# Optimization experiments

Measured on AMD Instinct MI355X. Metric: run time of the kernel, lower is better.

## Reference

```python
import jax, jax.numpy as jnp
import numpy as np

N, F, E = 2048, 4, 65536
D, H, FF = 256, 4, 2048  # d_model, n_heads, transformer feedforward dim
HD = D // H


def setup_inputs() -> dict:
    key = jax.random.key(0)
    ks = jax.random.split(key, 26)
    p = lambda k, shape, fan_in: (jax.random.normal(k, shape, jnp.float32) / np.sqrt(fan_in))
    return {
        "features": jax.random.normal(ks[0], (N, F), jnp.float32),
        "edges": jax.random.randint(ks[1], (2, E), 0, N, jnp.int64),
        # Embedder.linear: Linear(1, 256)
        "lin_w": p(ks[2], (D, 1), 1), "lin_b": jnp.zeros((D,), jnp.float32),
        # TransformerEncoderLayer self-attention
        "in_proj_w": p(ks[3], (3 * D, D), D), "in_proj_b": jnp.zeros((3 * D,), jnp.float32),
        "out_w": p(ks[4], (D, D), D), "out_b": jnp.zeros((D,), jnp.float32),
        "ln1_g": jnp.ones((D,), jnp.float32), "ln1_b": jnp.zeros((D,), jnp.float32),
        # feedforward
        "ffn_w1": p(ks[5], (FF, D), D), "ffn_b1": jnp.zeros((FF,), jnp.float32),
        "ffn_w2": p(ks[6], (D, FF), FF), "ffn_b2": jnp.zeros((D,), jnp.float32),
        "ln2_g": jnp.ones((D,), jnp.float32), "ln2_b": jnp.zeros((D,), jnp.float32),
        # 4 GCNConv layers (torch Linear convention: weight [out, in])
        "W1": p(ks[7], (512, D), D), "b1": jnp.zeros((512,), jnp.float32),
        "W2": p(ks[8], (512, 512), 512), "b2": jnp.zeros((512,), jnp.float32),
        "W3": p(ks[9], (512, 512), 512), "b3": jnp.zeros((512,), jnp.float32),
        "W4": p(ks[10], (512, 512), 512), "b4": jnp.zeros((512,), jnp.float32),
    }


def _layer_norm(x, g, b, eps=1e-5):
    m = jnp.mean(x, axis=-1, keepdims=True)
    v = jnp.mean((x - m) ** 2, axis=-1, keepdims=True)
    return (x - m) / jnp.sqrt(v + eps) * g + b


def _gcn_conv(x, W, b, src, dst, n):
    # PyG GCNConv: h = x @ W^T; add self-loops; norm = deg^-1/2[src]*deg^-1/2[dst];
    # out = scatter_add(norm * h[src] -> dst) + bias
    h = x @ W.T
    loop = jnp.arange(n, dtype=src.dtype)
    s = jnp.concatenate([src, loop])
    d = jnp.concatenate([dst, loop])
    deg = jax.ops.segment_sum(jnp.ones_like(d, dtype=h.dtype), d, num_segments=n)
    dinv = jnp.where(deg > 0, deg ** -0.5, 0.0)
    norm = dinv[s] * dinv[d]
    return jax.ops.segment_sum(h[s] * norm[:, None], d, num_segments=n) + b


def reference(features, edges, lin_w, lin_b, in_proj_w, in_proj_b, out_w, out_b,
              ln1_g, ln1_b, ffn_w1, ffn_b1, ffn_w2, ffn_b2, ln2_g, ln2_b,
              W1, b1, W2, b2, W3, b3, W4, b4):
    n, f = features.shape
    # Embedder: [N,F,1] -> Linear(1,D) -> [N,F,D]; seq-first transformer (seq=N, batch=F)
    x = features[..., None] @ lin_w.T + lin_b  # [N,F,D]
    qkv = x @ in_proj_w.T + in_proj_b          # [N,F,3D]
    q, k, v = jnp.split(qkv, 3, axis=-1)
    split = lambda t: t.reshape(n, f, H, HD).transpose(1, 2, 0, 3)  # [F,H,N,hd]
    q, k, v = split(q), split(k), split(v)
    scores = jnp.einsum('bhqd,bhkd->bhqk', q, k) / np.sqrt(HD)      # [F,H,N,N]
    attn = jax.nn.softmax(scores, axis=-1)
    o = jnp.einsum('bhqk,bhkd->bhqd', attn, v).transpose(2, 0, 1, 3).reshape(n, f, D)
    o = o @ out_w.T + out_b
    x = _layer_norm(x + o, ln1_g, ln1_b)
    ff = jax.nn.relu(x @ ffn_w1.T + ffn_b1) @ ffn_w2.T + ffn_b2
    x = _layer_norm(x + ff, ln2_g, ln2_b)
    x = jax.nn.relu(jnp.mean(x, axis=1))  # mean over feature-batch dim -> [N,D]

    src, dst = edges[0], edges[1]
    x = jax.nn.relu(_gcn_conv(x, W1, b1, src, dst, n))
    x = jax.nn.relu(_gcn_conv(x, W2, b2, src, dst, n))
    x = jax.nn.relu(_gcn_conv(x, W3, b3, src, dst, n))
    x = _gcn_conv(x, W4, b4, src, dst, n)
    return x
```

## Files before the change

kernel.cpp:

```cpp
#include <hip/hip_runtime.h>
#include <hip/hip_bf16.h>
#include <math.h>

#define NN   2048
#define FB   4
#define DD   256
#define EE   65536
#define NT   (NN*FB)
#define FFD  2048

typedef unsigned int u32;
typedef unsigned short u16;
typedef __attribute__((ext_vector_type(4))) float f32x4;
typedef __attribute__((ext_vector_type(8))) short bf16x8;

#define OFF_W2   0
#define OFF_G1   524288
#define OFF_G2   655360
#define OFF_G3   917504
#define OFF_G4   1179648
#define WBF_TOT  1441792

__device__ float g_A[768], g_B[768];
__device__ float g_coefA[4], g_coefC[4];
__device__ float g_meanv[6], g_G[36];
__device__ float g_Vx[8*DD];
__device__ u16   g_w1vh[FFD*8];
__device__ float g_m[NT*4];
__device__ float g_cc[NT*8];
__device__ u16   g_xmh[NN*DD];
__device__ u16   g_hsh[NN*512];
__device__ u16   g_xgh[NN*512];
__device__ u16   g_wbf[WBF_TOT];
__device__ __align__(64) int g_degp[NN*16];
__device__ __align__(64) int g_curp[NN*16];
__device__ int   g_off[NN+1], g_adj[EE];
__device__ float g_dinv[NN];

__device__ __forceinline__ u16 f2bf(float x) {
  u32 u = __float_as_uint(x);
  return (u16)((u + 0x7FFFu + ((u >> 16) & 1u)) >> 16);
}
__device__ __forceinline__ float bfl(u32 v) { return __uint_as_float(v << 16); }
__device__ __forceinline__ float bfh(u32 v) { return __uint_as_float(v & 0xffff0000u); }
__device__ __forceinline__ void gl_lds16(const void* g, void* l) {
  __builtin_amdgcn_global_load_lds(
      (const __attribute__((address_space(1))) u32*)g,
      (__attribute__((address_space(3))) u32*)l, 16, 0, 0);
}
__device__ __forceinline__ float qred(float v) {
  v += __shfl_xor(v, 1, 64);
  v += __shfl_xor(v, 2, 64);
  return v;
}
__device__ __forceinline__ void acc8(const uint4 v, float* a) {
  a[0]+=bfl(v.x); a[1]+=bfh(v.x);
  a[2]+=bfl(v.y); a[3]+=bfh(v.y);
  a[4]+=bfl(v.z); a[5]+=bfh(v.z);
  a[6]+=bfl(v.w); a[7]+=bfh(v.w);
}

__global__ __launch_bounds__(256) void k_fuse1(const float* __restrict__ ipw,
    const float* __restrict__ ipb, const float* __restrict__ linw,
    const float* __restrict__ linb) {
  __shared__ __align__(16) float sm[512];
  const int b = blockIdx.x, t = threadIdx.x;
  if (b < 12) {
    float* lw = sm; float* lb = sm + 256;
    lw[t] = linw[t]; lb[t] = linb[t];
    __syncthreads();
    int j = b*64 + (t>>2), c = t&3;
    const float4* row = (const float4*)&ipw[j*256 + c*64];
    float a = 0.f, bb = 0.f;
    #pragma unroll
    for (int q = 0; q < 16; q++) {
      float4 v = row[q]; int d0 = c*64 + q*4;
      a  += v.x*lw[d0] + v.y*lw[d0+1] + v.z*lw[d0+2] + v.w*lw[d0+3];
      bb += v.x*lb[d0] + v.y*lb[d0+1] + v.z*lb[d0+2] + v.w*lb[d0+3];
    }
    a = qred(a); bb = qred(bb);
    if (c == 0) { g_A[j] = a; g_B[j] = bb + ipb[j]; }
  } else {
    int i = (b - 12)*256 + t;
    if (i < NN*16) { g_degp[i] = 0; g_curp[i] = 0; }
  }
}

__global__ __launch_bounds__(256) void k_fuse2(const float* __restrict__ outw,
    const float* __restrict__ outb, const float* __restrict__ linw,
    const float* __restrict__ linb, const float* __restrict__ g1,
    const float* __restrict__ b1ln, const int* __restrict__ edges) {
  __shared__ __align__(16) float sm[512 + 4*27];
  const int b = blockIdx.x, t = threadIdx.x;
  if (b == 0) {
    int lane = t & 63, w = t >> 6;
    {
      float aq = g_A[w*64 + lane], ak = g_A[256 + w*64 + lane], bq = g_B[w*64 + lane];
      float pa = aq * ak, pc = bq * ak;
      #pragma unroll
      for (int o = 32; o > 0; o >>= 1) { pa += __shfl_down(pa, o, 64); pc += __shfl_down(pc, o, 64); }
      if (lane == 0) { g_coefA[w] = pa * 0.125f; g_coefC[w] = pc * 0.125f; }
    }
    float* A2 = sm; float* B2 = sm + 256; float* wred = sm + 512;
    A2[t] = g_A[512 + t]; B2[t] = g_B[512 + t];
    __syncthreads();
    const int d = t;
    const float4* row = (const float4*)&outw[d*256];
    float pv[4] = {0,0,0,0}, q0 = 0.f;
    #pragma unroll 8
    for (int q = 0; q < 64; q++) {
      float4 v = row[q]; int e0 = q*4; int h = q >> 4;
      pv[h] += v.x*A2[e0] + v.y*A2[e0+1] + v.z*A2[e0+2] + v.w*A2[e0+3];
      q0    += v.x*B2[e0] + v.y*B2[e0+1] + v.z*B2[e0+2] + v.w*B2[e0+3];
    }
    q0 += outb[d];
    float c0 = linb[d] + q0;
    float Mv[6] = { linw[d], pv[0], pv[1], pv[2], pv[3], c0 };
    float vals[27];
    { int idx = 0;
      #pragma unroll
      for (int k = 0; k < 6; k++) vals[idx++] = Mv[k];
      #pragma unroll
      for (int k = 0; k < 6; k++)
        #pragma unroll
        for (int l = 0; l < 6; l++) if (l >= k) vals[idx++] = Mv[k]*Mv[l];
    }
    #pragma unroll
    for (int k2 = 0; k2 < 27; k2++) {
      float v = vals[k2];
      #pragma unroll
      for (int o = 32; o > 0; o >>= 1) v += __shfl_down(v, o, 64);
      if (lane == 0) wred[w*27 + k2] = v;
    }
    __syncthreads();
    if (t < 27) {
      float s = wred[t] + wred[27 + t] + wred[54 + t] + wred[81 + t];
      if (t < 6) g_meanv[t] = s * (1.f/256.f);
      else {
        int p = t - 6, k = 0;
        while (p >= 6 - k) { p -= 6 - k; k++; }
        int l = k + p;
        g_G[k*6+l] = s; g_G[l*6+k] = s;
      }
    }
    #pragma unroll
    for (int k = 0; k < 6; k++) g_Vx[k*256 + d] = Mv[k] * g1[d];
    g_Vx[6*256 + d] = g1[d];
    g_Vx[7*256 + d] = b1ln[d];
  } else {
    int e = (b - 1)*256 + t;
    atomicAdd(&g_degp[edges[EE + e] * 16], 1);
  }
}

__global__ __launch_bounds__(256) void k_fuse3(const float* __restrict__ feat,
    const float* __restrict__ w1, const float* __restrict__ fb1,
    const float* __restrict__ w2c, const float* __restrict__ W1c,
    const float* __restrict__ W2c, const float* __restrict__ W3c,
    const float* __restrict__ W4c) {
  __shared__ __align__(16) char smraw[34816];
  const int b = blockIdx.x, t = threadIdx.x;
  if (b < 512) {
    float* fs = (float*)smraw;
    float* ss = fs + 8192;
    float* ww = ss + 256;
    for (int i = t; i < 2048; i += 256) {
      const float4 v = *(const float4*)&feat[i*4];
      fs[0*2048+i] = v.x; fs[1*2048+i] = v.y; fs[2*2048+i] = v.z; fs[3*2048+i] = v.w;
    }
    __syncthreads();
    int tuple = b * 64 + (t >> 2);
    int c = t & 3;
    int h = tuple & 3, f = (tuple >> 2) & 3, n = tuple >> 4;
    float fi = fs[f*2048 + n];
    float tt = g_coefA[h] * fi + g_coefC[h];
    float s = 0.f, wsum = 0.f;
    int j0 = c * 512;
    for (int j = j0; j < j0 + 512; j++) {
      float fj = fs[f*2048 + j];
      float e = __expf(tt * fj);
      s += e; wsum += e * fj;
    }
    ss[(t>>2)*4 + c] = s; ww[(t>>2)*4 + c] = wsum;
    __syncthreads();
    if (c == 0) {
      float S = ss[(t>>2)*4] + ss[(t>>2)*4+1] + ss[(t>>2)*4+2] + ss[(t>>2)*4+3];
      float W = ww[(t>>2)*4] + ww[(t>>2)*4+1] + ww[(t>>2)*4+2] + ww[(t>>2)*4+3];
      g_m[tuple] = W / S;
    }
  } else if (b < 544) {
    float* vx = (float*)smraw;
    #pragma unroll
    for (int k = 0; k < 8; k++) vx[k*256 + t] = g_Vx[k*256 + t];
    __syncthreads();
    int j = (b - 512)*64 + (t>>2), c = t&3;
    const float4* row = (const float4*)&w1[j*256 + c*64];
    float acc[8] = {0,0,0,0,0,0,0,0};
    #pragma unroll
    for (int q = 0; q < 16; q++) {
      float4 v = row[q]; int d0 = c*64 + q*4;
      #pragma unroll
      for (int k = 0; k < 8; k++)
        acc[k] += v.x*vx[k*256+d0] + v.y*vx[k*256+d0+1]
                + v.z*vx[k*256+d0+2] + v.w*vx[k*256+d0+3];
    }
    #pragma unroll
    for (int k = 0; k < 8; k++) acc[k] = qred(acc[k]);
    if (c == 0) {
      acc[7] += fb1[j];
      uint4 r;
      r.x = ((u32)f2bf(acc[1])<<16) | f2bf(acc[0]);
      r.y = ((u32)f2bf(acc[3])<<16) | f2bf(acc[2]);
      r.z = ((u32)f2bf(acc[5])<<16) | f2bf(acc[4]);
      r.w = ((u32)f2bf(acc[7])<<16) | f2bf(acc[6]);
      *(uint4*)&g_w1vh[j*8] = r;
    }
  } else if (b == 544) {
    int* wt = (int*)smraw;
    int base = t * 8;
    int v[8], ex[8], sum = 0;
    #pragma unroll
    for (int i = 0; i < 8; i++) { ex[i] = sum; v[i] = g_degp[(base+i)*16]; sum += v[i]; }
    int lane = t & 63, w = t >> 6;
    int inc = sum;
    #pragma unroll
    for (int o = 1; o < 64; o <<= 1) { int x = __shfl_up(inc, o, 64); if (lane >= o) inc += x; }
    if (lane == 63) wt[w] = inc;
    __syncthreads();
    int wb = 0;
    for (int j = 0; j < w; j++) wb += wt[j];
    int excl = wb + inc - sum;
    #pragma unroll
    for (int i = 0; i < 8; i++) {
      g_off[base+i] = excl + ex[i];
      g_dinv[base+i] = rsqrtf((float)(v[i] + 1));
    }
    if (t == 255) g_off[NN] = wb + inc;
  } else {
    int i = ((b - 545)*256 + t) * 4;
    const float* src; int off;
    if (i < OFF_G1)      { src = w2c; off = OFF_W2; }
    else if (i < OFF_G2) { src = W1c; off = OFF_G1; }
    else if (i < OFF_G3) { src = W2c; off = OFF_G2; }
    else if (i < OFF_G4) { src = W3c; off = OFF_G3; }
    else                 { src = W4c; off = OFF_G4; }
    float4 v = *(const float4*)&src[i - off];
    ushort4 r;
    r.x = f2bf(v.x); r.y = f2bf(v.y); r.z = f2bf(v.z); r.w = f2bf(v.w);
    *(ushort4*)&g_wbf[i] = r;
  }
}

__global__ __launch_bounds__(256) void k_fuse4(const float* __restrict__ feat,
                                               const int* __restrict__ edges) {
  const int b = blockIdx.x, t = threadIdx.x;
  if (b < 32) {
    int tok = b * 256 + t;
    int n = tok >> 2, f = tok & 3;
    float fi = feat[n*4 + f];
    float u[6] = { fi, g_m[tok*4+0], g_m[tok*4+1], g_m[tok*4+2], g_m[tok*4+3], 1.f };
    float mu = 0.f;
    #pragma unroll
    for (int k = 0; k < 6; k++) mu += g_meanv[k] * u[k];
    float q = 0.f;
    for (int k = 0; k < 6; k++)
      for (int l = 0; l < 6; l++) q += u[k] * g_G[k*6+l] * u[l];
    q *= (1.f/256.f);
    float var = q - mu * mu;
    float s = rsqrtf(var + 1e-5f);
    float4 w0; w0.x = fi*s; w0.y = u[1]*s; w0.z = u[2]*s; w0.w = u[3]*s;
    float4 w1v; w1v.x = u[4]*s; w1v.y = s; w1v.z = -mu*s; w1v.w = 1.f;
    *(float4*)&g_cc[tok*8]     = w0;
    *(float4*)&g_cc[tok*8 + 4] = w1v;
  } else {
    int e = (b - 32)*256 + t;
    int s = edges[e], d = edges[EE + e];
    int pos = atomicAdd(&g_curp[d*16], 1);
    g_adj[g_off[d] + pos] = s;
  }
}

__global__ __launch_bounds__(256) void k_ffnln(const float* __restrict__ fb2,
    const float* __restrict__ ln2g, const float* __restrict__ ln2b) {
  __shared__ __align__(16) char smp[74752];
  u16*   Bsl  = (u16*)smp;
  u16*   Asl  = (u16*)(smp + 65536);
  u16*   w1sl = (u16*)(smp + 69632);
  float* ccs  = (float*)(smp + 73728);
  float* part = (float*)(smp + 74240);

  const int b = blockIdx.x, t = threadIdx.x;
  const int w = t >> 6, lane = t & 63, fr = lane & 15, gk = lane >> 4;
  const int tok0 = b * 16;
  const u16* W2p = g_wbf + OFF_W2;

  if (t < 32) ((float4*)ccs)[t] = ((const float4*)&g_cc[tok0*8])[t];
  if (w == 1) {
    #pragma unroll
    for (int hh = 0; hh < 2; hh++) {
      int p = hh*64 + lane;
      int q = (p & ~7) | ((p ^ (p >> 3)) & 7);
      gl_lds16(g_w1vh + (size_t)q*8, w1sl + (hh << 9));
    }
  }
  __syncthreads();

  const int arow = t >> 4, aslot = t & 15;
  float ac[8];
  #pragma unroll
  for (int k = 0; k < 8; k++) ac[k] = ccs[arow*8 + k];

  f32x4 acc[4] = {};
  for (int it = 0; it < 16; it++) {
    const int k0 = it << 7;
    const int cur = it & 1;
    #pragma unroll
    for (int c = 0; c < 16; c++) {
      int col0 = (w << 6) + (c << 2);
      int colL = col0 + (lane >> 4);
      int p = lane & 15;
      int q = (p & 8) | ((p ^ (colL & 7)) & 7);
      gl_lds16(W2p + (size_t)colL*FFD + k0 + q*8, Bsl + (col0 << 7));
    }
    if (w == 1 && it < 15) {
      #pragma unroll
      for (int hh = 0; hh < 2; hh++) {
        int p = hh*64 + lane;
        int q = (p & ~7) | ((p ^ (p >> 3)) & 7);
        gl_lds16(g_w1vh + (size_t)(k0 + 128 + q)*8, w1sl + ((cur ^ 1) << 10) + (hh << 9));
      }
    }
    {
      float h[8];
      #pragma unroll
      for (int e2 = 0; e2 < 8; e2++) {
        int ph = aslot*8 + (e2 ^ (aslot & 7));
        uint4 wv = *(const uint4*)&w1sl[(cur << 10) + ph*8];
        float s = ac[0]*bfl(wv.x) + ac[1]*bfh(wv.x)
                + ac[2]*bfl(wv.y) + ac[3]*bfh(wv.y)
                + ac[4]*bfl(wv.z) + ac[5]*bfh(wv.z)
                + ac[6]*bfl(wv.w) + ac[7]*bfh(wv.w);
        h[e2] = fmaxf(s, 0.f);
      }
      uint4 r;
      r.x = ((u32)f2bf(h[1])<<16) | f2bf(h[0]);
      r.y = ((u32)f2bf(h[3])<<16) | f2bf(h[2]);
      r.z = ((u32)f2bf(h[5])<<16) | f2bf(h[4]);
      r.w = ((u32)f2bf(h[7])<<16) | f2bf(h[6]);
      int ph = (aslot & 8) | ((aslot ^ (arow & 7)) & 7);
      *(uint4*)&Asl[(arow << 7) + (ph << 3)] = r;
    }
    __syncthreads();
    #pragma unroll
    for (int kk = 0; kk < 4; kk++) {
      int qa = (kk << 2) + gk;
      int pa = (qa & 8) | ((qa ^ (fr & 7)) & 7);
      bf16x8 af = *(const bf16x8*)&Asl[(fr << 7) + (pa << 3)];
      #pragma unroll
      for (int nb = 0; nb < 4; nb++) {
        int col = (w << 6) + (nb << 4) + fr;
        int pb = (qa & 8) | ((qa ^ (col & 7)) & 7);
        bf16x8 bv = *(const bf16x8*)&Bsl[(col << 7) + (pb << 3)];
        acc[nb] = __builtin_amdgcn_mfma_f32_16x16x32_bf16(af, bv, acc[nb], 0, 0, 0);
      }
    }
    __syncthreads();
  }

  #pragma unroll
  for (int nb = 0; nb < 4; nb++) {
    int col = (w << 6) + (nb << 4) + fr;
    float fb = fb2[col];
    #pragma unroll
    for (int r = 0; r < 4; r++) {
      int row = gk*4 + r;
      float x1 = 0.f;
      #pragma unroll
      for (int k = 0; k < 8; k++) x1 += ccs[row*8 + k] * g_Vx[k*256 + col];
      acc[nb][r] += fb + x1;
    }
  }
  float s1[4] = {0,0,0,0}, s2v[4] = {0,0,0,0};
  #pragma unroll
  for (int r = 0; r < 4; r++)
    #pragma unroll
    for (int nb = 0; nb < 4; nb++) {
      float v = acc[nb][r];
      s1[r] += v; s2v[r] += v*v;
    }
  #pragma unroll
  for (int o = 1; o < 16; o <<= 1) {
    #pragma unroll
    for (int r = 0; r < 4; r++) {
      s1[r]  += __shfl_xor(s1[r],  o, 64);
      s2v[r] += __shfl_xor(s2v[r], o, 64);
    }
  }
  if (fr == 0) {
    #pragma unroll
    for (int r = 0; r < 4; r++) {
      int row = gk*4 + r;
      part[(w*16 + row)*2 + 0] = s1[r];
      part[(w*16 + row)*2 + 1] = s2v[r];
    }
  }
  __syncthreads();
  float mu[4], inv[4];
  #pragma unroll
  for (int r = 0; r < 4; r++) {
    int row = gk*4 + r;
    float S1 = 0.f, S2 = 0.f;
    #pragma unroll
    for (int wv = 0; wv < 4; wv++) {
      S1 += part[(wv*16 + row)*2 + 0];
      S2 += part[(wv*16 + row)*2 + 1];
    }
    float m = S1 * (1.f/256.f);
    mu[r] = m;
    inv[r] = rsqrtf(S2 * (1.f/256.f) - m*m + 1e-5f);
  }
  const int node = b*4 + gk;
  #pragma unroll
  for (int nb = 0; nb < 4; nb++) {
    int col = (w << 6) + (nb << 4) + fr;
    float g = ln2g[col], bb = ln2b[col];
    float m = 0.f;
    #pragma unroll
    for (int r = 0; r < 4; r++)
      m += (acc[nb][r] - mu[r]) * inv[r] * g + bb;
    g_xmh[node*256 + col] = f2bf(fmaxf(m * 0.25f, 0.f));
  }
}

template<int DO_ROWSCALE, int OUT_BF16, int HAS_BIAS>
__global__ __launch_bounds__(256) void k_mm64(
    const u16* __restrict__ A, const u16* __restrict__ Bm, void* __restrict__ Cv,
    int M, int N, int K,
    const float* __restrict__ rowscale, const float* __restrict__ bias)
{
  __shared__ u16 Asl[32*64];
  __shared__ u16 Bsl[64*64];
  const int t = threadIdx.x;
  const int w = t >> 6, lane = t & 63;
  const int bm = blockIdx.y * 32, bn = blockIdx.x * 64;
  const int wr = w >> 1, wc = w & 1;
  const int fr = lane & 15;
  const int gk = lane >> 4;
  f32x4 acc[2] = {};
  for (int k0 = 0; k0 < K; k0 += 64) {
    {
      int r = (w << 3) + (lane >> 3);
      int ks = (((lane & 7) ^ (r & 7)) << 3);
      gl_lds16(A + (size_t)(bm + r)*K + k0 + ks, Asl + (w << 9));
    }
    #pragma unroll
    for (int c = 0; c < 2; c++) {
      int r2 = (w << 4) + (c << 3) + (lane >> 3);
      int ks2 = (((lane & 7) ^ (r2 & 7)) << 3);
      gl_lds16(Bm + (size_t)(bn + r2)*K + k0 + ks2, Bsl + (w << 10) + (c << 9));
    }
    __syncthreads();
    bf16x8 af[2], bfv[2][2];
    #pragma unroll
    for (int kk = 0; kk < 2; kk++) {
      int q = (kk << 2) + gk;
      int row = wr*16 + fr;
      af[kk] = *(const bf16x8*)&Asl[(row << 6) + ((q ^ (row & 7)) << 3)];
    }
    #pragma unroll
    for (int nb = 0; nb < 2; nb++) {
      int col = wc*32 + nb*16 + fr;
      #pragma unroll
      for (int kk = 0; kk < 2; kk++) {
        int q = (kk << 2) + gk;
        bfv[nb][kk] = *(const bf16x8*)&Bsl[(col << 6) + ((q ^ (col & 7)) << 3)];
      }
    }
    #pragma unroll
    for (int kk = 0; kk < 2; kk++)
      #pragma unroll
      for (int nb = 0; nb < 2; nb++)
        acc[nb] = __builtin_amdgcn_mfma_f32_16x16x32_bf16(af[kk], bfv[nb][kk], acc[nb], 0, 0, 0);
    __syncthreads();
  }
  #pragma unroll
  for (int r = 0; r < 4; r++) {
    int row = bm + wr*16 + gk*4 + r;
    float rs = DO_ROWSCALE ? rowscale[row] : 1.f;
    #pragma unroll
    for (int nb = 0; nb < 2; nb++) {
      int col = bn + wc*32 + nb*16 + fr;
      float v = acc[nb][r];
      if (HAS_BIAS) v += bias[col];
      if (DO_ROWSCALE) v *= rs;
      if (OUT_BF16) ((u16*)Cv)[(size_t)row*N + col] = f2bf(v);
      else ((float*)Cv)[(size_t)row*N + col] = v;
    }
  }
}

template<int OUT_BF16, int DO_RELU>
__global__ __launch_bounds__(256) void k_agg(const float* __restrict__ bias,
                                             void* __restrict__ outv) {
  const int t = threadIdx.x, w = t >> 6, lane = t & 63;
  const int i = blockIdx.x*4 + w;
  const int d = lane * 8;
  const uint4* tbl = (const uint4*)g_hsh;
  float a[8] = {0,0,0,0,0,0,0,0};
  acc8(tbl[i*64 + lane], a);
  int e0 = g_off[i], e1 = g_off[i+1];
  int e = e0;
  for (; e + 4 <= e1; e += 4) {
    int s0 = g_adj[e+0], s1 = g_adj[e+1], s2 = g_adj[e+2], s3 = g_adj[e+3];
    uint4 v0 = tbl[s0*64 + lane];
    uint4 v1 = tbl[s1*64 + lane];
    uint4 v2 = tbl[s2*64 + lane];
    uint4 v3 = tbl[s3*64 + lane];
    acc8(v0, a); acc8(v1, a); acc8(v2, a); acc8(v3, a);
  }
  for (; e < e1; e++) acc8(tbl[g_adj[e]*64 + lane], a);
  float di = g_dinv[i];
  const float4 b0 = *(const float4*)&bias[d];
  const float4 b1 = *(const float4*)&bias[d+4];
  a[0]=di*a[0]+b0.x; a[1]=di*a[1]+b0.y; a[2]=di*a[2]+b0.z; a[3]=di*a[3]+b0.w;
  a[4]=di*a[4]+b1.x; a[5]=di*a[5]+b1.y; a[6]=di*a[6]+b1.z; a[7]=di*a[7]+b1.w;
  if (DO_RELU) {
    #pragma unroll
    for (int q = 0; q < 8; q++) a[q] = fmaxf(a[q], 0.f);
  }
  if (OUT_BF16) {
    uint4 r;
    r.x = ((u32)f2bf(a[1])<<16) | f2bf(a[0]);
    r.y = ((u32)f2bf(a[3])<<16) | f2bf(a[2]);
    r.z = ((u32)f2bf(a[5])<<16) | f2bf(a[4]);
    r.w = ((u32)f2bf(a[7])<<16) | f2bf(a[6]);
    *(uint4*)&((u16*)outv)[i*512 + d] = r;
  } else {
    float4 r0; r0.x=a[0]; r0.y=a[1]; r0.z=a[2]; r0.w=a[3];
    float4 r1; r1.x=a[4]; r1.y=a[5]; r1.z=a[6]; r1.w=a[7];
    *(float4*)&((float*)outv)[i*512 + d]     = r0;
    *(float4*)&((float*)outv)[i*512 + d + 4] = r1;
  }
}

static float* symf(const void* s) { void* p = nullptr; (void)hipGetSymbolAddress(&p, s); return (float*)p; }

extern "C" void kernel_launch(void* const* d_in, const int* in_sizes, int n_in,
                              void* d_out, int out_size, void* d_ws, size_t ws_size,
                              hipStream_t stream) {
  const float* feat = (const float*)d_in[0];
  const int*   edges= (const int*)  d_in[1];
  const float* linw = (const float*)d_in[2];
  const float* linb = (const float*)d_in[3];
  const float* ipw  = (const float*)d_in[4];
  const float* ipb  = (const float*)d_in[5];
  const float* outw = (const float*)d_in[6];
  const float* outb = (const float*)d_in[7];
  const float* ln1g = (const float*)d_in[8];
  const float* ln1b = (const float*)d_in[9];
  const float* fw1  = (const float*)d_in[10];
  const float* fb1  = (const float*)d_in[11];
  const float* fw2  = (const float*)d_in[12];
  const float* fb2  = (const float*)d_in[13];
  const float* ln2g = (const float*)d_in[14];
  const float* ln2b = (const float*)d_in[15];
  const float* W1g  = (const float*)d_in[16];
  const float* b1g  = (const float*)d_in[17];
  const float* W2g  = (const float*)d_in[18];
  const float* b2g  = (const float*)d_in[19];
  const float* W3g  = (const float*)d_in[20];
  const float* b3g  = (const float*)d_in[21];
  const float* W4g  = (const float*)d_in[22];
  const float* b4g  = (const float*)d_in[23];
  float* out = (float*)d_out;

  u16*   p_xmh = (u16*)symf(HIP_SYMBOL(g_xmh));
  u16*   p_hsh = (u16*)symf(HIP_SYMBOL(g_hsh));
  u16*   p_xgh = (u16*)symf(HIP_SYMBOL(g_xgh));
  u16*   p_wbf = (u16*)symf(HIP_SYMBOL(g_wbf));
  float* p_dinv= symf(HIP_SYMBOL(g_dinv));

  k_fuse1<<<140,  256, 0, stream>>>(ipw, ipb, linw, linb);
  k_fuse2<<<257,  256, 0, stream>>>(outw, outb, linw, linb, ln1g, ln1b, edges);
  k_fuse3<<<1953, 256, 0, stream>>>(feat, fw1, fb1, fw2, W1g, W2g, W3g, W4g);
  k_fuse4<<<288,  256, 0, stream>>>(feat, edges);

  k_ffnln<<<512, 256, 0, stream>>>(fb2, ln2g, ln2b);

  k_mm64<1,1,0><<<dim3(8, 64), 256, 0, stream>>>(
      p_xmh, p_wbf + OFF_G1, p_hsh, NN, 512, 256, p_dinv, nullptr);
  k_agg<1,1><<<NN/4, 256, 0, stream>>>(b1g, p_xgh);
  k_mm64<1,1,0><<<dim3(8, 64), 256, 0, stream>>>(
      p_xgh, p_wbf + OFF_G2, p_hsh, NN, 512, 512, p_dinv, nullptr);
  k_agg<1,1><<<NN/4, 256, 0, stream>>>(b2g, p_xgh);
  k_mm64<1,1,0><<<dim3(8, 64), 256, 0, stream>>>(
      p_xgh, p_wbf + OFF_G3, p_hsh, NN, 512, 512, p_dinv, nullptr);
  k_agg<1,1><<<NN/4, 256, 0, stream>>>(b3g, p_xgh);
  k_mm64<1,1,0><<<dim3(8, 64), 256, 0, stream>>>(
      p_xgh, p_wbf + OFF_G4, p_hsh, NN, 512, 512, p_dinv, nullptr);
  k_agg<0,0><<<NN/4, 256, 0, stream>>>(b4g, out);
}
```

Measured before the change: 166.4 us.

## Retile FFN to 64-token by 128-column blocks and split LayerNorm into separate kernel

The fused FFN+LayerNorm kernel is replaced by one that processes 64 tokens by 128 output columns per block (256 blocks instead of 512). The whole W1 vector table is preloaded into LDS, and each W2 tile load is reused across four times more tokens. Because the 256 LN columns are now split across two blocks, the kernel writes fp32 pre-norm activations and partial sums to global memory. A new k_ln2m kernel then applies LayerNorm2, the feature mean and ReLU. This cuts redundant W2 traffic and W1 reloads but adds an 8 MB fp32 round trip, an extra launch, fewer blocks, and larger LDS use per block.

```diff
diff --git a/kernel.cpp b/kernel.cpp
--- a/kernel.cpp
+++ b/kernel.cpp
@@ -28,6 +28,8 @@
 __device__ u16   g_w1vh[FFD*8];
 __device__ float g_m[NT*4];
 __device__ float g_cc[NT*8];
+__device__ float g_ffv[(size_t)NT*DD];
+__device__ float g_lnp[NT*2*2];
 __device__ u16   g_xmh[NN*DD];
 __device__ u16   g_hsh[NN*512];
 __device__ u16   g_xgh[NN*512];
@@ -280,86 +282,84 @@
   }
 }
 
-__global__ __launch_bounds__(256) void k_ffnln(const float* __restrict__ fb2,
-    const float* __restrict__ ln2g, const float* __restrict__ ln2b) {
-  __shared__ __align__(16) char smp[74752];
+__global__ __launch_bounds__(256) void k_ffn(const float* __restrict__ fb2) {
+  __shared__ __align__(16) char smp[88576];
   u16*   Bsl  = (u16*)smp;
-  u16*   Asl  = (u16*)(smp + 65536);
-  u16*   w1sl = (u16*)(smp + 69632);
-  float* ccs  = (float*)(smp + 73728);
-  float* part = (float*)(smp + 74240);
+  u16*   Asl  = (u16*)(smp + 32768);
+  u16*   w1s  = (u16*)(smp + 49152);
+  float* ccs  = (float*)(smp + 81920);
+  float* vxs  = (float*)(smp + 83968);
+  float* fb2s = (float*)(smp + 88064);
 
   const int b = blockIdx.x, t = threadIdx.x;
   const int w = t >> 6, lane = t & 63, fr = lane & 15, gk = lane >> 4;
-  const int tok0 = b * 16;
+  const int tb = b >> 1, ch = b & 1;
+  const int tok0 = tb * 64, gc0 = ch * 128;
   const u16* W2p = g_wbf + OFF_W2;
 
-  if (t < 32) ((float4*)ccs)[t] = ((const float4*)&g_cc[tok0*8])[t];
-  if (w == 1) {
-    #pragma unroll
-    for (int hh = 0; hh < 2; hh++) {
-      int p = hh*64 + lane;
-      int q = (p & ~7) | ((p ^ (p >> 3)) & 7);
-      gl_lds16(g_w1vh + (size_t)q*8, w1sl + (hh << 9));
-    }
-  }
+  #pragma unroll
+  for (int q = 0; q < 8; q++) {
+    int jj = t + q*256;
+    uint4 v = *(const uint4*)&g_w1vh[jj*8];
+    int idx = (jj & ~7) | ((jj ^ (jj >> 3)) & 7);
+    *(uint4*)&w1s[idx*8] = v;
+  }
+  if (t < 128) ((float4*)ccs)[t] = ((const float4*)&g_cc[tok0*8])[t];
+  { int k = t >> 5, c4 = t & 31;
+    ((float4*)vxs)[t] = *(const float4*)&g_Vx[k*256 + gc0 + c4*4]; }
+  if (t < 32) ((float4*)fb2s)[t] = *(const float4*)&fb2[gc0 + t*4];
   __syncthreads();
 
-  const int arow = t >> 4, aslot = t & 15;
+  const int arow = t >> 2;
+  const int sb = (t & 3) * 4;
   float ac[8];
   #pragma unroll
   for (int k = 0; k < 8; k++) ac[k] = ccs[arow*8 + k];
 
-  f32x4 acc[4] = {};
+  f32x4 acc[8] = {};
   for (int it = 0; it < 16; it++) {
     const int k0 = it << 7;
-    const int cur = it & 1;
-    #pragma unroll
-    for (int c = 0; c < 16; c++) {
-      int col0 = (w << 6) + (c << 2);
+    #pragma unroll
+    for (int c = 0; c < 8; c++) {
+      int col0 = (w << 5) + (c << 2);
       int colL = col0 + (lane >> 4);
       int p = lane & 15;
       int q = (p & 8) | ((p ^ (colL & 7)) & 7);
-      gl_lds16(W2p + (size_t)colL*FFD + k0 + q*8, Bsl + (col0 << 7));
-    }
-    if (w == 1 && it < 15) {
-      #pragma unroll
-      for (int hh = 0; hh < 2; hh++) {
-        int p = hh*64 + lane;
-        int q = (p & ~7) | ((p ^ (p >> 3)) & 7);
-        gl_lds16(g_w1vh + (size_t)(k0 + 128 + q)*8, w1sl + ((cur ^ 1) << 10) + (hh << 9));
-      }
-    }
-    {
+      gl_lds16(W2p + (size_t)(gc0 + colL)*FFD + k0 + q*8, Bsl + (col0 << 7));
+    }
+    #pragma unroll
+    for (int sj = 0; sj < 4; sj++) {
+      int s = sb + sj;
       float h[8];
       #pragma unroll
       for (int e2 = 0; e2 < 8; e2++) {
-        int ph = aslot*8 + (e2 ^ (aslot & 7));
-        uint4 wv = *(const uint4*)&w1sl[(cur << 10) + ph*8];
-        float s = ac[0]*bfl(wv.x) + ac[1]*bfh(wv.x)
-                + ac[2]*bfl(wv.y) + ac[3]*bfh(wv.y)
-                + ac[4]*bfl(wv.z) + ac[5]*bfh(wv.z)
-                + ac[6]*bfl(wv.w) + ac[7]*bfh(wv.w);
-        h[e2] = fmaxf(s, 0.f);
+        int idx = (k0 + s*8) + (e2 ^ (s & 7));
+        uint4 wv = *(const uint4*)&w1s[idx*8];
+        float sv = ac[0]*bfl(wv.x) + ac[1]*bfh(wv.x)
+                 + ac[2]*bfl(wv.y) + ac[3]*bfh(wv.y)
+                 + ac[4]*bfl(wv.z) + ac[5]*bfh(wv.z)
+                 + ac[6]*bfl(wv.w) + ac[7]*bfh(wv.w);
+        h[e2] = fmaxf(sv, 0.f);
       }
       uint4 r;
       r.x = ((u32)f2bf(h[1])<<16) | f2bf(h[0]);
       r.y = ((u32)f2bf(h[3])<<16) | f2bf(h[2]);
       r.z = ((u32)f2bf(h[5])<<16) | f2bf(h[4]);
       r.w = ((u32)f2bf(h[7])<<16) | f2bf(h[6]);
-      int ph = (aslot & 8) | ((aslot ^ (arow & 7)) & 7);
-      *(uint4*)&Asl[(arow << 7) + (ph << 3)] = r;
+      int p = (s & 8) | ((s ^ (arow & 7)) & 7);
+      *(uint4*)&Asl[(arow << 7) + (p << 3)] = r;
     }
     __syncthreads();
     #pragma unroll
     for (int kk = 0; kk < 4; kk++) {
-      int qa = (kk << 2) + gk;
-      int pa = (qa & 8) | ((qa ^ (fr & 7)) & 7);
-      bf16x8 af = *(const bf16x8*)&Asl[(fr << 7) + (pa << 3)];
-      #pragma unroll
-      for (int nb = 0; nb < 4; nb++) {
-        int col = (w << 6) + (nb << 4) + fr;
-        int pb = (qa & 8) | ((qa ^ (col & 7)) & 7);
+      int s = (kk << 2) + gk;
+      int row = (w << 4) + fr;
+      int pa = (s & 8) | ((s ^ (row & 7)) & 7);
+      bf16x8 af = *(const bf16x8*)&Asl[(row << 7) + (pa << 3)];
+      #pragma unroll
+      for (int nb = 0; nb < 8; nb++) {
+        int col = (nb << 4) + fr;
+        int pb = (s & 8) | ((s ^ (col & 7)) & 7);
         bf16x8 bv = *(const bf16x8*)&Bsl[(col << 7) + (pb << 3)];
         acc[nb] = __builtin_amdgcn_mfma_f32_16x16x32_bf16(af, bv, acc[nb], 0, 0, 0);
       }
@@ -367,68 +367,78 @@
     __syncthreads();
   }
 
+  float s1[4] = {0,0,0,0}, s2[4] = {0,0,0,0};
   #pragma unroll
-  for (int nb = 0; nb < 4; nb++) {
-    int col = (w << 6) + (nb << 4) + fr;
-    float fb = fb2[col];
+  for (int nb = 0; nb < 8; nb++) {
+    int lcol = (nb << 4) + fr;
+    float fb = fb2s[lcol];
     #pragma unroll
     for (int r = 0; r < 4; r++) {
-      int row = gk*4 + r;
+      int lrow = (w << 4) + gk*4 + r;
       float x1 = 0.f;
       #pragma unroll
-      for (int k = 0; k < 8; k++) x1 += ccs[row*8 + k] * g_Vx[k*256 + col];
-      acc[nb][r] += fb + x1;
-    }
-  }
-  float s1[4] = {0,0,0,0}, s2v[4] = {0,0,0,0};
-  #pragma unroll
-  for (int r = 0; r < 4; r++)
-    #pragma unroll
-    for (int nb = 0; nb < 4; nb++) {
-      float v = acc[nb][r];
-      s1[r] += v; s2v[r] += v*v;
-    }
+      for (int k = 0; k < 8; k++) x1 += ccs[lrow*8 + k] * vxs[k*128 + lcol];
+      float v = acc[nb][r] + fb + x1;
+      s1[r] += v; s2[r] += v*v;
+      g_ffv[(size_t)(tok0 + lrow)*256 + gc0 + lcol] = v;
+    }
+  }
   #pragma unroll
   for (int o = 1; o < 16; o <<= 1) {
     #pragma unroll
     for (int r = 0; r < 4; r++) {
-      s1[r]  += __shfl_xor(s1[r],  o, 64);
-      s2v[r] += __shfl_xor(s2v[r], o, 64);
+      s1[r] += __shfl_xor(s1[r], o, 64);
+      s2[r] += __shfl_xor(s2[r], o, 64);
     }
   }
   if (fr == 0) {
     #pragma unroll
     for (int r = 0; r < 4; r++) {
-      int row = gk*4 + r;
-      part[(w*16 + row)*2 + 0] = s1[r];
-      part[(w*16 + row)*2 + 1] = s2v[r];
-    }
-  }
-  __syncthreads();
-  float mu[4], inv[4];
-  #pragma unroll
-  for (int r = 0; r < 4; r++) {
-    int row = gk*4 + r;
-    float S1 = 0.f, S2 = 0.f;
-    #pragma unroll
-    for (int wv = 0; wv < 4; wv++) {
-      S1 += part[(wv*16 + row)*2 + 0];
-      S2 += part[(wv*16 + row)*2 + 1];
-    }
-    float m = S1 * (1.f/256.f);
-    mu[r] = m;
-    inv[r] = rsqrtf(S2 * (1.f/256.f) - m*m + 1e-5f);
-  }
-  const int node = b*4 + gk;
-  #pragma unroll
-  for (int nb = 0; nb < 4; nb++) {
-    int col = (w << 6) + (nb << 4) + fr;
-    float g = ln2g[col], bb = ln2b[col];
-    float m = 0.f;
-    #pragma unroll
-    for (int r = 0; r < 4; r++)
-      m += (acc[nb][r] - mu[r]) * inv[r] * g + bb;
-    g_xmh[node*256 + col] = f2bf(fmaxf(m * 0.25f, 0.f));
+      int tok = tok0 + (w << 4) + gk*4 + r;
+      g_lnp[(tok*2 + ch)*2 + 0] = s1[r];
+      g_lnp[(tok*2 + ch)*2 + 1] = s2[r];
+    }
+  }
+}
+
+__global__ __launch_bounds__(256) void k_ln2m(const float* __restrict__ ln2g,
+                                              const float* __restrict__ ln2b) {
+  __shared__ __align__(16) float xs[4*256];
+  const int b = blockIdx.x, t = threadIdx.x;
+  const int f = t >> 6, lane = t & 63;
+  const int d0 = lane * 4;
+  for (int qn = 0; qn < 4; qn++) {
+    int n = b*4 + qn;
+    int tok = n*4 + f;
+    float4 v = *(const float4*)&g_ffv[(size_t)tok*256 + d0];
+    float S1 = g_lnp[(tok*2+0)*2+0] + g_lnp[(tok*2+1)*2+0];
+    float S2 = g_lnp[(tok*2+0)*2+1] + g_lnp[(tok*2+1)*2+1];
+    float mu = S1 * (1.f/256.f);
+    float var = S2 * (1.f/256.f) - mu*mu;
+    float inv = rsqrtf(var + 1e-5f);
+    float4 gg = *(const float4*)&ln2g[d0];
+    float4 bb = *(const float4*)&ln2b[d0];
+    float4 x2;
+    x2.x = (v.x-mu)*inv*gg.x + bb.x;
+    x2.y = (v.y-mu)*inv*gg.y + bb.y;
+    x2.z = (v.z-mu)*inv*gg.z + bb.z;
+    x2.w = (v.w-mu)*inv*gg.w + bb.w;
+    *(float4*)&xs[f*256 + d0] = x2;
+    __syncthreads();
+    if (t < 64) {
+      int dd = t * 4;
+      float4 a0 = *(const float4*)&xs[0*256 + dd];
+      float4 a1 = *(const float4*)&xs[1*256 + dd];
+      float4 a2 = *(const float4*)&xs[2*256 + dd];
+      float4 a3 = *(const float4*)&xs[3*256 + dd];
+      ushort4 r;
+      r.x = f2bf(fmaxf((a0.x+a1.x+a2.x+a3.x)*0.25f, 0.f));
+      r.y = f2bf(fmaxf((a0.y+a1.y+a2.y+a3.y)*0.25f, 0.f));
+      r.z = f2bf(fmaxf((a0.z+a1.z+a2.z+a3.z)*0.25f, 0.f));
+      r.w = f2bf(fmaxf((a0.w+a1.w+a2.w+a3.w)*0.25f, 0.f));
+      *(ushort4*)&g_xmh[n*256 + dd] = r;
+    }
+    __syncthreads();
   }
 }
 
@@ -585,7 +595,8 @@
   k_fuse3<<<1953, 256, 0, stream>>>(feat, fw1, fb1, fw2, W1g, W2g, W3g, W4g);
   k_fuse4<<<288,  256, 0, stream>>>(feat, edges);
 
-  k_ffnln<<<512, 256, 0, stream>>>(fb2, ln2g, ln2b);
+  k_ffn <<<256, 256, 0, stream>>>(fb2);
+  k_ln2m<<<NN/4, 256, 0, stream>>>(ln2g, ln2b);
 
   k_mm64<1,1,0><<<dim3(8, 64), 256, 0, stream>>>(
       p_xmh, p_wbf + OFF_G1, p_hsh, NN, 512, 256, p_dinv, nullptr);
```

New measurement: 185.4 us. 11.4% more time.

## Double FFN token tile per block to halve W2 tile reloads

Applied to the files above, without the earlier changes.

The fused FFN+LayerNorm kernel now handles 32 tokens per block instead of 16, with each wave holding two row-blocks of MFMA accumulators. Each W2 tile staged in LDS is reused across twice as many rows, which halves the total W2 traffic from global/L2 and halves the grid to 256 blocks. The trade-off is more LDS, more accumulator registers and only 256 blocks, roughly one per CU, which leaves less latency hiding.

```diff
diff --git a/kernel.cpp b/kernel.cpp
--- a/kernel.cpp
+++ b/kernel.cpp
@@ -282,19 +282,19 @@
 
 __global__ __launch_bounds__(256) void k_ffnln(const float* __restrict__ fb2,
     const float* __restrict__ ln2g, const float* __restrict__ ln2b) {
-  __shared__ __align__(16) char smp[74752];
+  __shared__ __align__(16) char smp[79872];
   u16*   Bsl  = (u16*)smp;
   u16*   Asl  = (u16*)(smp + 65536);
-  u16*   w1sl = (u16*)(smp + 69632);
-  float* ccs  = (float*)(smp + 73728);
-  float* part = (float*)(smp + 74240);
+  u16*   w1sl = (u16*)(smp + 73728);
+  float* ccs  = (float*)(smp + 77824);
+  float* part = (float*)(smp + 78848);
 
   const int b = blockIdx.x, t = threadIdx.x;
   const int w = t >> 6, lane = t & 63, fr = lane & 15, gk = lane >> 4;
-  const int tok0 = b * 16;
+  const int tok0 = b * 32;
   const u16* W2p = g_wbf + OFF_W2;
 
-  if (t < 32) ((float4*)ccs)[t] = ((const float4*)&g_cc[tok0*8])[t];
+  if (t < 64) ((float4*)ccs)[t] = ((const float4*)&g_cc[tok0*8])[t];
   if (w == 1) {
     #pragma unroll
     for (int hh = 0; hh < 2; hh++) {
@@ -305,12 +305,13 @@
   }
   __syncthreads();
 
-  const int arow = t >> 4, aslot = t & 15;
+  const int arow = t >> 3;
+  const int sb = (t & 7) * 2;
   float ac[8];
   #pragma unroll
   for (int k = 0; k < 8; k++) ac[k] = ccs[arow*8 + k];
 
-  f32x4 acc[4] = {};
+  f32x4 acc[2][4] = {};
   for (int it = 0; it < 16; it++) {
     const int k0 = it << 7;
     const int cur = it & 1;
@@ -330,105 +331,124 @@
         gl_lds16(g_w1vh + (size_t)(k0 + 128 + q)*8, w1sl + ((cur ^ 1) << 10) + (hh << 9));
       }
     }
-    {
+    #pragma unroll
+    for (int sj = 0; sj < 2; sj++) {
+      int s = sb + sj;
       float h[8];
       #pragma unroll
       for (int e2 = 0; e2 < 8; e2++) {
-        int ph = aslot*8 + (e2 ^ (aslot & 7));
+        int ph = s*8 + (e2 ^ (s & 7));
         uint4 wv = *(const uint4*)&w1sl[(cur << 10) + ph*8];
-        float s = ac[0]*bfl(wv.x) + ac[1]*bfh(wv.x)
-                + ac[2]*bfl(wv.y) + ac[3]*bfh(wv.y)
-                + ac[4]*bfl(wv.z) + ac[5]*bfh(wv.z)
-                + ac[6]*bfl(wv.w) + ac[7]*bfh(wv.w);
-        h[e2] = fmaxf(s, 0.f);
+        float sv = ac[0]*bfl(wv.x) + ac[1]*bfh(wv.x)
+                 + ac[2]*bfl(wv.y) + ac[3]*bfh(wv.y)
+                 + ac[4]*bfl(wv.z) + ac[5]*bfh(wv.z)
+                 + ac[6]*bfl(wv.w) + ac[7]*bfh(wv.w);
+        h[e2] = fmaxf(sv, 0.f);
       }
       uint4 r;
       r.x = ((u32)f2bf(h[1])<<16) | f2bf(h[0]);
       r.y = ((u32)f2bf(h[3])<<16) | f2bf(h[2]);
       r.z = ((u32)f2bf(h[5])<<16) | f2bf(h[4]);
       r.w = ((u32)f2bf(h[7])<<16) | f2bf(h[6]);
-      int ph = (aslot & 8) | ((aslot ^ (arow & 7)) & 7);
+      int ph = (s & 8) | ((s ^ (arow & 7)) & 7);
       *(uint4*)&Asl[(arow << 7) + (ph << 3)] = r;
     }
     __syncthreads();
     #pragma unroll
     for (int kk = 0; kk < 4; kk++) {
       int qa = (kk << 2) + gk;
-      int pa = (qa & 8) | ((qa ^ (fr & 7)) & 7);
-      bf16x8 af = *(const bf16x8*)&Asl[(fr << 7) + (pa << 3)];
+      #pragma unroll
+      for (int rb = 0; rb < 2; rb++) {
+        int row = rb*16 + fr;
+        int pa = (qa & 8) | ((qa ^ (row & 7)) & 7);
+        bf16x8 af = *(const bf16x8*)&Asl[(row << 7) + (pa << 3)];
+        #pragma unroll
+        for (int nb = 0; nb < 4; nb++) {
+          int col = (w << 6) + (nb << 4) + fr;
+          int pb = (qa & 8) | ((qa ^ (col & 7)) & 7);
+          bf16x8 bv = *(const bf16x8*)&Bsl[(col << 7) + (pb << 3)];
+          acc[rb][nb] = __builtin_amdgcn_mfma_f32_16x16x32_bf16(af, bv, acc[rb][nb], 0, 0, 0);
+        }
+      }
+    }
+    __syncthreads();
+  }
+
+  #pragma unroll
+  for (int rb = 0; rb < 2; rb++)
+    #pragma unroll
+    for (int nb = 0; nb < 4; nb++) {
+      int col = (w << 6) + (nb << 4) + fr;
+      float fb = fb2[col];
+      #pragma unroll
+      for (int r = 0; r < 4; r++) {
+        int row = rb*16 + gk*4 + r;
+        float x1 = 0.f;
+        #pragma unroll
+        for (int k = 0; k < 8; k++) x1 += ccs[row*8 + k] * g_Vx[k*256 + col];
+        acc[rb][nb][r] += fb + x1;
+      }
+    }
+  float s1[2][4] = {}, s2v[2][4] = {};
+  #pragma unroll
+  for (int rb = 0; rb < 2; rb++)
+    #pragma unroll
+    for (int r = 0; r < 4; r++)
       #pragma unroll
       for (int nb = 0; nb < 4; nb++) {
-        int col = (w << 6) + (nb << 4) + fr;
-        int pb = (qa & 8) | ((qa ^ (col & 7)) & 7);
-        bf16x8 bv = *(const bf16x8*)&Bsl[(col << 7) + (pb << 3)];
-        acc[nb] = __builtin_amdgcn_mfma_f32_16x16x32_bf16(af, bv, acc[nb], 0, 0, 0);
-      }
-    }
-    __syncthreads();
-  }
-
-  #pragma unroll
-  for (int nb = 0; nb < 4; nb++) {
-    int col = (w << 6) + (nb << 4) + fr;
-    float fb = fb2[col];
-    #pragma unroll
-    for (int r = 0; r < 4; r++) {
-      int row = gk*4 + r;
-      float x1 = 0.f;
-      #pragma unroll
-      for (int k = 0; k < 8; k++) x1 += ccs[row*8 + k] * g_Vx[k*256 + col];
-      acc[nb][r] += fb + x1;
-    }
-  }
-  float s1[4] = {0,0,0,0}, s2v[4] = {0,0,0,0};
-  #pragma unroll
-  for (int r = 0; r < 4; r++)
-    #pragma unroll
-    for (int nb = 0; nb < 4; nb++) {
-      float v = acc[nb][r];
-      s1[r] += v; s2v[r] += v*v;
-    }
+        float v = acc[rb][nb][r];
+        s1[rb][r] += v; s2v[rb][r] += v*v;
+      }
   #pragma unroll
   for (int o = 1; o < 16; o <<= 1) {
     #pragma unroll
+    for (int rb = 0; rb < 2; rb++)
+      #pragma unroll
+      for (int r = 0; r < 4; r++) {
+        s1[rb][r]  += __shfl_xor(s1[rb][r],  o, 64);
+        s2v[rb][r] += __shfl_xor(s2v[rb][r], o, 64);
+      }
+  }
+  if (fr == 0) {
+    #pragma unroll
+    for (int rb = 0; rb < 2; rb++)
+      #pragma unroll
+      for (int r = 0; r < 4; r++) {
+        int row = rb*16 + gk*4 + r;
+        part[(w*32 + row)*2 + 0] = s1[rb][r];
+        part[(w*32 + row)*2 + 1] = s2v[rb][r];
+      }
+  }
+  __syncthreads();
+  float mu[2][4], inv[2][4];
+  #pragma unroll
+  for (int rb = 0; rb < 2; rb++)
+    #pragma unroll
     for (int r = 0; r < 4; r++) {
-      s1[r]  += __shfl_xor(s1[r],  o, 64);
-      s2v[r] += __shfl_xor(s2v[r], o, 64);
-    }
-  }
-  if (fr == 0) {
-    #pragma unroll
-    for (int r = 0; r < 4; r++) {
-      int row = gk*4 + r;
-      part[(w*16 + row)*2 + 0] = s1[r];
-      part[(w*16 + row)*2 + 1] = s2v[r];
-    }
-  }
-  __syncthreads();
-  float mu[4], inv[4];
+      int row = rb*16 + gk*4 + r;
+      float S1 = 0.f, S2 = 0.f;
+      #pragma unroll
+      for (int wv = 0; wv < 4; wv++) {
+        S1 += part[(wv*32 + row)*2 + 0];
+        S2 += part[(wv*32 + row)*2 + 1];
+      }
+      float m = S1 * (1.f/256.f);
+      mu[rb][r] = m;
+      inv[rb][r] = rsqrtf(S2 * (1.f/256.f) - m*m + 1e-5f);
+    }
   #pragma unroll
-  for (int r = 0; r < 4; r++) {
-    int row = gk*4 + r;
-    float S1 = 0.f, S2 = 0.f;
-    #pragma unroll
-    for (int wv = 0; wv < 4; wv++) {
-      S1 += part[(wv*16 + row)*2 + 0];
-      S2 += part[(wv*16 + row)*2 + 1];
-    }
-    float m = S1 * (1.f/256.f);
-    mu[r] = m;
-    inv[r] = rsqrtf(S2 * (1.f/256.f) - m*m + 1e-5f);
-  }
-  const int node = b*4 + gk;
-  #pragma unroll
-  for (int nb = 0; nb < 4; nb++) {
-    int col = (w << 6) + (nb << 4) + fr;
-    float g = ln2g[col], bb = ln2b[col];
-    float m = 0.f;
-    #pragma unroll
-    for (int r = 0; r < 4; r++)
-      m += (acc[nb][r] - mu[r]) * inv[r] * g + bb;
-    g_xmh[node*256 + col] = f2bf(fmaxf(m * 0.25f, 0.f));
+  for (int rb = 0; rb < 2; rb++) {
+    int node = b*8 + rb*4 + gk;
+    #pragma unroll
+    for (int nb = 0; nb < 4; nb++) {
+      int col = (w << 6) + (nb << 4) + fr;
+      float g = ln2g[col], bb = ln2b[col];
+      float m = 0.f;
+      #pragma unroll
+      for (int r = 0; r < 4; r++)
+        m += (acc[rb][nb][r] - mu[rb][r]) * inv[rb][r] * g + bb;
+      g_xmh[node*256 + col] = f2bf(fmaxf(m * 0.25f, 0.f));
+    }
   }
 }
 
@@ -585,7 +605,7 @@
   k_fuse3<<<1953, 256, 0, stream>>>(feat, fw1, fb1, fw2, W1g, W2g, W3g, W4g);
   k_fuse4<<<288,  256, 0, stream>>>(feat, edges);
 
-  k_ffnln<<<512, 256, 0, stream>>>(fb2, ln2g, ln2b);
+  k_ffnln<<<256, 256, 0, stream>>>(fb2, ln2g, ln2b);
 
   k_mm64<1,1,0><<<dim3(8, 64), 256, 0, stream>>>(
       p_xmh, p_wbf + OFF_G1, p_hsh, NN, 512, 256, p_dinv, nullptr);
```

Measured after the change: 175.7 us. 5.6% more time.
